# Optimization experiments

Measured on AMD Instinct MI355X. Metric: run time of the kernel, lower is better.

Reference implementation:

```python
import jax, jax.numpy as jnp
import numpy as np

D_MODEL = 512
N_HEADS = 8
D_K = D_MODEL // N_HEADS
D_FF = 2048
N = 4096
EPS = 1e-5


def _layer_norm(x, g, b):
    mu = jnp.mean(x, axis=-1, keepdims=True)
    var = jnp.mean(jnp.square(x - mu), axis=-1, keepdims=True)
    return (x - mu) * jax.lax.rsqrt(var + EPS) * g + b


def setup_inputs() -> dict:
    key = jax.random.key(0)
    ks = jax.random.split(key, 16)
    s = 1.0 / np.sqrt(D_MODEL)
    sf = 1.0 / np.sqrt(D_FF)
    inp = {
        "h": jax.random.normal(ks[0], (N, D_MODEL), dtype=jnp.float32),
        "adj": jax.random.randint(ks[1], (N, N), 0, 2, dtype=jnp.int32),
        "Wq": jax.random.uniform(ks[2], (D_MODEL, D_MODEL), jnp.float32, -s, s),
        "bq": jnp.zeros((D_MODEL,), jnp.float32),
        "Wk": jax.random.uniform(ks[3], (D_MODEL, D_MODEL), jnp.float32, -s, s),
        "bk": jnp.zeros((D_MODEL,), jnp.float32),
        "Wv": jax.random.uniform(ks[4], (D_MODEL, D_MODEL), jnp.float32, -s, s),
        "bv": jnp.zeros((D_MODEL,), jnp.float32),
        "Wo": jax.random.uniform(ks[5], (D_MODEL, D_MODEL), jnp.float32, -s, s),
        "bo": jnp.zeros((D_MODEL,), jnp.float32),
        "W1": jax.random.uniform(ks[6], (D_FF, D_MODEL), jnp.float32, -s, s),
        "b1": jnp.zeros((D_FF,), jnp.float32),
        "W2": jax.random.uniform(ks[7], (D_MODEL, D_FF), jnp.float32, -sf, sf),
        "b2": jnp.zeros((D_MODEL,), jnp.float32),
        "ln1_g": jnp.ones((D_MODEL,), jnp.float32),
        "ln1_b": jnp.zeros((D_MODEL,), jnp.float32),
        "ln2_g": jnp.ones((D_MODEL,), jnp.float32),
        "ln2_b": jnp.zeros((D_MODEL,), jnp.float32),
    }
    return inp


def reference(h, adj, Wq, bq, Wk, bk, Wv, bv, Wo, bo, W1, b1, W2, b2,
              ln1_g, ln1_b, ln2_g, ln2_b):
    n = h.shape[0]
    # adjacency + self loops, used as attention mask (batch=1)
    mask = adj.astype(jnp.float32) + jnp.eye(n, dtype=jnp.float32)  # [N,N]

    # QKV projections, split into heads: [N, H, Dk]
    q = (h @ Wq.T + bq).reshape(n, N_HEADS, D_K)
    k = (h @ Wk.T + bk).reshape(n, N_HEADS, D_K)
    v = (h @ Wv.T + bv).reshape(n, N_HEADS, D_K)

    scores = jnp.einsum("nhd,mhd->hnm", q, k) / jnp.sqrt(jnp.float32(D_K))
    scores = jnp.where(mask[None, :, :] == 0, jnp.float32(-1e9), scores)
    attn = jax.nn.softmax(scores, axis=-1)  # dropout is identity in eval
    ctx = jnp.einsum("hnm,mhd->nhd", attn, v).reshape(n, D_MODEL)
    attn_out = ctx @ Wo.T + bo

    h1 = _layer_norm(h + attn_out, ln1_g, ln1_b)
    ff = jax.nn.relu(h1 @ W1.T + b1) @ W2.T + b2
    h2 = _layer_norm(h1 + ff, ln2_g, ln2_b)
    return h2
```

## Files before the change

### kernel.cpp

```cpp
#include <hip/hip_runtime.h>
#include <stdint.h>
#include <stddef.h>

typedef __bf16 bf16;
typedef __bf16 bf16x8 __attribute__((ext_vector_type(8)));
typedef float  f32x4  __attribute__((ext_vector_type(4)));

typedef __attribute__((address_space(3))) void       lds_void;
typedef __attribute__((address_space(1))) const void gbl_cvoid;

#define ASYNC_CP16(g, l) \
  __builtin_amdgcn_global_load_lds((gbl_cvoid*)(g), (lds_void*)(l), 16, 0, 0)

__device__ __forceinline__ int swz(int r) { return (r & 7) ^ ((r & 8) >> 1); }

struct CastArgs {
  const float* src[7];
  bf16*        dst[7];
  int          cum[8];
};

__global__ __launch_bounds__(256) void k_prep(
    const int* __restrict__ adj, unsigned long long* __restrict__ mb,
    CastArgs a, int total8)
{
  const int bid = blockIdx.x;
  if (bid < 65536) {
    const int gw   = (int)(((unsigned)bid * 256 + threadIdx.x) >> 6);
    const int lane = threadIdx.x & 63;
    const int av   = adj[(size_t)gw * 64 + lane];
    unsigned long long m = __ballot(av != 0);
    const int row = gw >> 6, wc = gw & 63;
    if ((row >> 6) == wc) m |= 1ull << (row & 63);
    if (lane == 0) mb[gw] = m;
  } else {
    const int g = (bid - 65536) * 256 + threadIdx.x;
    if (g >= total8) return;
    int t = 0;
    while (a.cum[t + 1] <= g) ++t;
    const int i = g - a.cum[t];
    const float4* s = (const float4*)(a.src[t]) + (size_t)i * 2;
    const float4 x0 = s[0], x1 = s[1];
    bf16x8 y;
    y[0] = (bf16)x0.x; y[1] = (bf16)x0.y; y[2] = (bf16)x0.z; y[3] = (bf16)x0.w;
    y[4] = (bf16)x1.x; y[5] = (bf16)x1.y; y[6] = (bf16)x1.z; y[7] = (bf16)x1.w;
    *(bf16x8*)(a.dst[t] + (size_t)i * 8) = y;
  }
}

template <int MT>
__device__ __forceinline__ void gemm_core_async(
    const bf16* __restrict__ A, const bf16* __restrict__ B,
    bf16* As, bf16* Bs, f32x4 (&acc)[4][(MT == 128) ? 4 : 2],
    int K, int m0, int n0, int kbeg, int kend)
{
  constexpr int FN = (MT == 128) ? 4 : 2;
  constexpr int IA = MT / 32;
  const int tid    = threadIdx.x;
  const int lane   = tid & 63;
  const int wave   = tid >> 6;
  const int lane15 = lane & 15;
  const int quad   = lane >> 4;
  const int wm     = (MT == 128) ? ((wave & 1) << 6) : 0;
  const int wn     = (MT == 128) ? ((wave >> 1) << 6) : (wave << 5);

  int srA[IA], soA[IA], srB[4], soB[4];
#pragma unroll
  for (int i = 0; i < IA; ++i) {
    int c  = ((wave * IA + i) << 6) + lane;
    srA[i] = c >> 3;
    soA[i] = ((c & 7) ^ swz(srA[i])) * 8;
  }
#pragma unroll
  for (int i = 0; i < 4; ++i) {
    int c  = ((wave * 4 + i) << 6) + lane;
    srB[i] = c >> 3;
    soB[i] = ((c & 7) ^ swz(srB[i])) * 8;
  }

  const bf16* Ab = A + (size_t)m0 * K;
  const bf16* Bb = B + (size_t)n0 * K;

  for (int k0 = kbeg; k0 < kend; k0 += 64) {
#pragma unroll
    for (int i = 0; i < IA; ++i)
      ASYNC_CP16(Ab + (size_t)srA[i] * K + k0 + soA[i], &As[(wave * IA + i) * 512]);
#pragma unroll
    for (int i = 0; i < 4; ++i)
      ASYNC_CP16(Bb + (size_t)srB[i] * K + k0 + soB[i], &Bs[(wave * 4 + i) * 512]);
    __syncthreads();

#pragma unroll
    for (int kk = 0; kk < 2; ++kk) {
      bf16x8 af[4], bfr[FN];
#pragma unroll
      for (int f = 0; f < 4; ++f) {
        const int ra = wm + f * 16 + lane15;
        af[f] = *(const bf16x8*)&As[ra * 64 + (((kk * 4 + quad) ^ swz(ra)) * 8)];
      }
#pragma unroll
      for (int f = 0; f < FN; ++f) {
        const int rb = wn + f * 16 + lane15;
        bfr[f] = *(const bf16x8*)&Bs[rb * 64 + (((kk * 4 + quad) ^ swz(rb)) * 8)];
      }
#pragma unroll
      for (int fm = 0; fm < 4; ++fm)
#pragma unroll
        for (int fn = 0; fn < FN; ++fn)
          acc[fm][fn] = __builtin_amdgcn_mfma_f32_16x16x32_bf16(
              af[fm], bfr[fn], acc[fm][fn], 0, 0, 0);
    }
    __syncthreads();
  }
}

__global__ __launch_bounds__(256, 2) void k_gemm(
    const bf16* __restrict__ A, const bf16* __restrict__ B,
    const float* __restrict__ bias, bf16* __restrict__ C,
    int N, int K, int relu)
{
  __shared__ __align__(16) bf16 As[128 * 64];
  __shared__ __align__(16) bf16 Bs[128 * 64];
  const int m0 = blockIdx.x * 128, n0 = blockIdx.y * 128;
  f32x4 acc[4][4] = {};
  gemm_core_async<128>(A, B, As, Bs, acc, K, m0, n0, 0, K);

  const int lane15 = threadIdx.x & 15;
  const int quad   = (threadIdx.x & 63) >> 4;
  const int wave   = threadIdx.x >> 6;
  const int wm = (wave & 1) << 6, wn = (wave >> 1) << 6;
#pragma unroll
  for (int fm = 0; fm < 4; ++fm)
#pragma unroll
    for (int fn = 0; fn < 4; ++fn) {
      const int col = n0 + wn + fn * 16 + lane15;
      const float bv = bias[col];
#pragma unroll
      for (int r = 0; r < 4; ++r) {
        const int row = m0 + wm + fm * 16 + quad * 4 + r;
        float v = acc[fm][fn][r] + bv;
        if (relu) v = fmaxf(v, 0.0f);
        C[(size_t)row * N + col] = (bf16)v;
      }
    }
}

__global__ __launch_bounds__(256, 4) void k_gemm_qkv(
    const bf16* __restrict__ h, const bf16* __restrict__ Wcat,
    const float* __restrict__ bq, const float* __restrict__ bk,
    const float* __restrict__ bv,
    bf16* __restrict__ q, bf16* __restrict__ k, bf16* __restrict__ vt)
{
  __shared__ __align__(16) bf16 SM[64 * 64 + 128 * 64];
  bf16* As = SM;
  bf16* Bs = SM + 64 * 64;
  const int m0 = blockIdx.x * 64, n0 = blockIdx.y * 128;
  f32x4 acc[4][2] = {};
  gemm_core_async<64>(h, Wcat, As, Bs, acc, 512, m0, n0, 0, 512);

  const int lane15 = threadIdx.x & 15;
  const int quad   = (threadIdx.x & 63) >> 4;
  const int wave   = threadIdx.x >> 6;
  const int wn     = wave << 5;
  const int proj   = n0 >> 9;
  const int ncol0  = n0 & 511;
  const float* bias = (proj == 0) ? bq : (proj == 1) ? bk : bv;

  if (proj < 2) {
    bf16* C = proj ? k : q;
#pragma unroll
    for (int fm = 0; fm < 4; ++fm)
#pragma unroll
      for (int fn = 0; fn < 2; ++fn) {
        const int col = ncol0 + wn + fn * 16 + lane15;
        const float bvv = bias[col];
#pragma unroll
        for (int r = 0; r < 4; ++r) {
          const int row = m0 + fm * 16 + quad * 4 + r;
          C[(size_t)row * 512 + col] = (bf16)(acc[fm][fn][r] + bvv);
        }
      }
  } else {
    __syncthreads();
#pragma unroll
    for (int fm = 0; fm < 4; ++fm)
#pragma unroll
      for (int fn = 0; fn < 2; ++fn) {
        const int colL = wn + fn * 16 + lane15;
        const float bvv = bias[ncol0 + colL];
#pragma unroll
        for (int r = 0; r < 4; ++r) {
          const int rowL = fm * 16 + quad * 4 + r;
          SM[colL * 72 + rowL] = (bf16)(acc[fm][fn][r] + bvv);
        }
      }
    __syncthreads();
#pragma unroll
    for (int i = 0; i < 4; ++i) {
      const int c = i * 256 + threadIdx.x;
      const int colL = c >> 3, rw = (c & 7) * 8;
      *(bf16x8*)&vt[(size_t)(ncol0 + colL) * 4096 + m0 + rw] =
          *(const bf16x8*)&SM[colL * 72 + rw];
    }
  }
}

__global__ __launch_bounds__(256, 4) void k_gemm_sk(
    const bf16* __restrict__ A, const bf16* __restrict__ B,
    float* __restrict__ Cp, int N, int K, int Ksplit)
{
  __shared__ __align__(16) bf16 As[64 * 64];
  __shared__ __align__(16) bf16 Bs[128 * 64];
  const int m0 = blockIdx.x * 64, n0 = blockIdx.y * 128;
  const int kbeg = blockIdx.z * Ksplit;
  f32x4 acc[4][2] = {};
  gemm_core_async<64>(A, B, As, Bs, acc, K, m0, n0, kbeg, kbeg + Ksplit);

  const int lane15 = threadIdx.x & 15;
  const int quad   = (threadIdx.x & 63) >> 4;
  const int wave   = threadIdx.x >> 6;
  const int wn     = wave << 5;
  float* Cz = Cp + (size_t)blockIdx.z * 4096 * N;
#pragma unroll
  for (int fm = 0; fm < 4; ++fm)
#pragma unroll
    for (int fn = 0; fn < 2; ++fn) {
      const int col = n0 + wn + fn * 16 + lane15;
#pragma unroll
      for (int r = 0; r < 4; ++r) {
        const int row = m0 + fm * 16 + quad * 4 + r;
        Cz[(size_t)row * N + col] = acc[fm][fn][r];
      }
    }
}

__global__ __launch_bounds__(256, 4) void k_attn(
    const bf16* __restrict__ Q, const bf16* __restrict__ Km,
    const bf16* __restrict__ Vt, const unsigned long long* __restrict__ mb,
    bf16* __restrict__ Opart, float* __restrict__ Lpart)
{
  constexpr int PP = 68;
  __shared__ __align__(16) bf16 Ks[64 * 64];
  __shared__ __align__(16) bf16 Vs[64 * 64];
  __shared__ __align__(16) bf16 Plb[4][32 * PP];

  const int tid    = threadIdx.x;
  const int wave   = tid >> 6;
  const int lane   = tid & 63;
  const int lane15 = lane & 15;
  const int quad   = lane >> 4;
  const int sp     = blockIdx.x & 3;
  const int hd     = (blockIdx.x >> 2) & 7;
  const int qt     = blockIdx.x >> 5;
  const int qrow   = qt * 128 + wave * 32;

  bf16x8 qf[2][2];
#pragma unroll
  for (int mt = 0; mt < 2; ++mt)
#pragma unroll
    for (int c = 0; c < 2; ++c)
      qf[mt][c] = *(const bf16x8*)&Q[(size_t)(qrow + mt * 16 + lane15) * 512 +
                                     hd * 64 + c * 32 + quad * 8];

  int srK[2], soK[2];
#pragma unroll
  for (int i = 0; i < 2; ++i) {
    int c  = ((wave * 2 + i) << 6) + lane;
    srK[i] = c >> 3;
    soK[i] = ((c & 7) ^ swz(srK[i])) * 8;
  }
  const bf16* KmB[2] = {
      Km + (size_t)srK[0] * 512 + hd * 64 + soK[0],
      Km + (size_t)srK[1] * 512 + hd * 64 + soK[1]};
  const bf16* VtB[2] = {
      Vt + (size_t)(hd * 64 + srK[0]) * 4096 + soK[0],
      Vt + (size_t)(hd * 64 + srK[1]) * 4096 + soK[1]};

  bf16x8 ones;
#pragma unroll
  for (int j = 0; j < 8; ++j) ones[j] = (bf16)1.0f;

  f32x4 o[2][4] = {};
  f32x4 la[2]   = {};

  const int kt0 = sp * 16;
#pragma unroll
  for (int i = 0; i < 2; ++i)
    ASYNC_CP16(KmB[i] + (size_t)(kt0 * 64) * 512, &Ks[(wave * 2 + i) * 512]);
  __syncthreads();

  for (int kt = kt0; kt < kt0 + 16; ++kt) {
    const int kb = kt * 64;

#pragma unroll
    for (int i = 0; i < 2; ++i)
      ASYNC_CP16(VtB[i] + kb, &Vs[(wave * 2 + i) * 512]);

    unsigned long long mw[2][4];
#pragma unroll
    for (int mt = 0; mt < 2; ++mt)
#pragma unroll
      for (int r = 0; r < 4; ++r)
        mw[mt][r] = mb[(size_t)(qrow + mt * 16 + quad * 4 + r) * 64 + kt] >> lane15;

#pragma unroll
    for (int g = 0; g < 4; ++g) {
      const int row = g * 16 + lane15;
      bf16x8 k0f = *(const bf16x8*)&Ks[row * 64 + ((quad       ^ swz(row)) * 8)];
      bf16x8 k1f = *(const bf16x8*)&Ks[row * 64 + (((4 + quad) ^ swz(row)) * 8)];
#pragma unroll
      for (int mt = 0; mt < 2; ++mt) {
        f32x4 s = {};
        __builtin_amdgcn_s_setprio(1);
        s = __builtin_amdgcn_mfma_f32_16x16x32_bf16(qf[mt][0], k0f, s, 0, 0, 0);
        s = __builtin_amdgcn_mfma_f32_16x16x32_bf16(qf[mt][1], k1f, s, 0, 0, 0);
        __builtin_amdgcn_s_setprio(0);
#pragma unroll
        for (int r = 0; r < 4; ++r) {
          const bool ok = ((mw[mt][r] >> (g * 16)) & 1ull) != 0;
          const float p = ok ? __expf(s[r] * 0.125f) : 0.0f;
          Plb[wave][(mt * 16 + quad * 4 + r) * PP + g * 16 + lane15] = (bf16)p;
        }
      }
    }
    __syncthreads();

    if (kt + 1 < kt0 + 16) {
      const int kb2 = (kt + 1) * 64;
#pragma unroll
      for (int i = 0; i < 2; ++i)
        ASYNC_CP16(KmB[i] + (size_t)kb2 * 512, &Ks[(wave * 2 + i) * 512]);
    }

#pragma unroll
    for (int c2 = 0; c2 < 2; ++c2) {
      bf16x8 vf[4];
#pragma unroll
      for (int g2 = 0; g2 < 4; ++g2) {
        const int row = g2 * 16 + lane15;
        vf[g2] = *(const bf16x8*)&Vs[row * 64 + (((c2 * 4 + quad) ^ swz(row)) * 8)];
      }
#pragma unroll
      for (int mt = 0; mt < 2; ++mt) {
        bf16x8 pa = *(const bf16x8*)&Plb[wave][(mt * 16 + lane15) * PP + c2 * 32 + quad * 8];
        __builtin_amdgcn_s_setprio(1);
        la[mt] = __builtin_amdgcn_mfma_f32_16x16x32_bf16(pa, ones, la[mt], 0, 0, 0);
#pragma unroll
        for (int g2 = 0; g2 < 4; ++g2)
          o[mt][g2] = __builtin_amdgcn_mfma_f32_16x16x32_bf16(pa, vf[g2], o[mt][g2], 0, 0, 0);
        __builtin_amdgcn_s_setprio(0);
      }
    }
    __syncthreads();
  }

  bf16* Oz = Opart + (size_t)sp * 4096 * 512;
#pragma unroll
  for (int mt = 0; mt < 2; ++mt) {
#pragma unroll
    for (int g2 = 0; g2 < 4; ++g2)
#pragma unroll
      for (int r = 0; r < 4; ++r) {
        const int row = qrow + mt * 16 + quad * 4 + r;
        Oz[(size_t)row * 512 + hd * 64 + g2 * 16 + lane15] = (bf16)o[mt][g2][r];
      }
    if (lane15 == 0) {
#pragma unroll
      for (int r = 0; r < 4; ++r)
        Lpart[sp * 32768 + (qrow + mt * 16 + quad * 4 + r) * 8 + hd] = la[mt][r];
    }
  }
}

__global__ __launch_bounds__(256) void k_attn_combine(
    const bf16* __restrict__ Opart, const float* __restrict__ Lpart,
    bf16* __restrict__ ctx)
{
  const int g = blockIdx.x * 256 + threadIdx.x;
  const size_t base = (size_t)g * 8;
  const int row = g >> 6;
  const int hd  = (g & 63) >> 3;
  float acc[8] = {};
  float l = 0.0f;
#pragma unroll
  for (int s = 0; s < 4; ++s) {
    bf16x8 ov = *(const bf16x8*)&Opart[(size_t)s * 4096 * 512 + base];
#pragma unroll
    for (int j = 0; j < 8; ++j) acc[j] += (float)ov[j];
    l += Lpart[s * 32768 + row * 8 + hd];
  }
  const float rl = 1.0f / l;
  bf16x8 y;
#pragma unroll
  for (int j = 0; j < 8; ++j) y[j] = (bf16)(acc[j] * rl);
  *(bf16x8*)(ctx + base) = y;
}

template <int F32OUT>
__global__ __launch_bounds__(256) void k_addln_sk(
    const bf16* __restrict__ x, const float* __restrict__ Cp,
    const float* __restrict__ bias,
    const float* __restrict__ gam, const float* __restrict__ bet,
    void* __restrict__ out)
{
  const int wave = threadIdx.x >> 6, lane = threadIdx.x & 63;
  const int row  = blockIdx.x * 4 + wave;
  const size_t base = (size_t)row * 512 + lane * 8;
  const int col = lane * 8;
  bf16x8 xv = *(const bf16x8*)(x + base);
  const float* p0 = Cp + base;
  const float* p1 = Cp + (size_t)4096 * 512 + base;
  f32x4 a0 = *(const f32x4*)p0, a1 = *(const f32x4*)(p0 + 4);
  f32x4 b0 = *(const f32x4*)p1, b1 = *(const f32x4*)(p1 + 4);
  f32x4 c0 = *(const f32x4*)(bias + col), c1 = *(const f32x4*)(bias + col + 4);
  float v[8], s = 0.0f, s2 = 0.0f;
#pragma unroll
  for (int j = 0; j < 4; ++j) {
    v[j]     = (float)xv[j]     + a0[j] + b0[j] + c0[j];
    v[4 + j] = (float)xv[4 + j] + a1[j] + b1[j] + c1[j];
  }
#pragma unroll
  for (int j = 0; j < 8; ++j) { s += v[j]; s2 += v[j] * v[j]; }
#pragma unroll
  for (int d = 1; d < 64; d <<= 1) { s += __shfl_xor(s, d, 64); s2 += __shfl_xor(s2, d, 64); }
  const float mu  = s * (1.0f / 512.0f);
  const float var = s2 * (1.0f / 512.0f) - mu * mu;
  const float rs  = rsqrtf(var + 1e-5f);
  f32x4 g0 = *(const f32x4*)(gam + col), g1 = *(const f32x4*)(gam + col + 4);
  f32x4 e0 = *(const f32x4*)(bet + col), e1 = *(const f32x4*)(bet + col + 4);
  if (F32OUT) {
    float* o = (float*)out + base;
#pragma unroll
    for (int j = 0; j < 4; ++j) {
      o[j]     = ((v[j] - mu) * rs) * g0[j] + e0[j];
      o[4 + j] = ((v[4 + j] - mu) * rs) * g1[j] + e1[j];
    }
  } else {
    bf16x8 ov;
#pragma unroll
    for (int j = 0; j < 4; ++j) {
      ov[j]     = (bf16)(((v[j] - mu) * rs) * g0[j] + e0[j]);
      ov[4 + j] = (bf16)(((v[4 + j] - mu) * rs) * g1[j] + e1[j]);
    }
    *(bf16x8*)((bf16*)out + base) = ov;
  }
}

extern "C" void kernel_launch(void* const* d_in, const int* in_sizes, int n_in,
                              void* d_out, int out_size, void* d_ws, size_t ws_size,
                              hipStream_t stream)
{
  const int*   adj = (const int*)  d_in[1];
  const float* bq  = (const float*)d_in[3];
  const float* bk  = (const float*)d_in[5];
  const float* bv  = (const float*)d_in[7];
  const float* bo  = (const float*)d_in[9];
  const float* b1  = (const float*)d_in[11];
  const float* b2  = (const float*)d_in[13];
  const float* g1  = (const float*)d_in[14];
  const float* be1 = (const float*)d_in[15];
  const float* g2  = (const float*)d_in[16];
  const float* be2 = (const float*)d_in[17];

  char* ws = (char*)d_ws;
  const size_t MB = 1024 * 1024;

  bf16* hb  = (bf16*)(ws + 0 * MB);
  bf16* Wqb = (bf16*)(ws + 4 * MB);
  bf16* Wkb = (bf16*)(ws + 4 * MB + 512 * 1024);
  bf16* Wvb = (bf16*)(ws + 5 * MB);
  bf16* Wob = (bf16*)(ws + 5 * MB + 512 * 1024);
  bf16* W1b = (bf16*)(ws + 6 * MB);
  bf16* W2b = (bf16*)(ws + 8 * MB);

  bf16* q    = (bf16*)(ws + 12 * MB);
  bf16* k    = (bf16*)(ws + 16 * MB);
  bf16* vt   = (bf16*)(ws + 24 * MB);
  unsigned long long* mbits = (unsigned long long*)(ws + 28 * MB);
  bf16* ctx  = (bf16*)(ws + 30 * MB);
  bf16*  Opart = (bf16*)(ws + 34 * MB);
  float* Lpart = (float*)(ws + 50 * MB);
  float* skP   = (float*)(ws + 34 * MB);
  bf16* h1   = (bf16*)(ws + 12 * MB);
  bf16* ff1  = (bf16*)(ws + 16 * MB);

  CastArgs ca;
  const int srcIdx[7] = {0, 2, 4, 6, 8, 10, 12};
  bf16* dsts[7] = {hb, Wqb, Wkb, Wvb, Wob, W1b, W2b};
  int cum = 0;
  for (int t = 0; t < 7; ++t) {
    ca.src[t] = (const float*)d_in[srcIdx[t]];
    ca.dst[t] = dsts[t];
    ca.cum[t] = cum;
    cum += in_sizes[srcIdx[t]] / 8;
  }
  ca.cum[7] = cum;

  const dim3 blk(256);

  k_prep<<<dim3(65536 + (cum + 255) / 256), blk, 0, stream>>>(adj, mbits, ca, cum);
  k_gemm_qkv<<<dim3(64, 12), blk, 0, stream>>>(hb, Wqb, bq, bk, bv, q, k, vt);
  k_attn<<<dim3(1024), blk, 0, stream>>>(q, k, vt, mbits, Opart, Lpart);
  k_attn_combine<<<dim3(1024), blk, 0, stream>>>(Opart, Lpart, ctx);
  k_gemm_sk<<<dim3(64, 4, 2), blk, 0, stream>>>(ctx, Wob, skP, 512, 512, 256);
  k_addln_sk<0><<<dim3(1024), blk, 0, stream>>>(hb, skP, bo, g1, be1, (void*)h1);
  k_gemm<<<dim3(32, 16), blk, 0, stream>>>(h1, W1b, b1, ff1, 2048, 512, 1);
  k_gemm_sk<<<dim3(64, 4, 2), blk, 0, stream>>>(ff1, W2b, skP, 512, 2048, 1024);
  k_addln_sk<1><<<dim3(1024), blk, 0, stream>>>(h1, skP, b2, g2, be2, d_out);
}
```

Before: 294.0 us.

## Restructure attention K/V loading, prefetch mask bits, swizzle P tile, coalesce output

Reworks the attention inner loop so that K and V tiles are loaded together at the top of each iteration, followed by one barrier. The mask words for the next tile are prefetched into registers while the current tile is computed. The P scratch tile now uses a row pitch of 72 plus an XOR swizzle to avoid LDS bank conflicts, and exp is computed with exp2 and a folded scale. The output is staged through LDS so each lane writes 16-byte vectors instead of scattered bf16 stores. The cost is that the K load is no longer overlapped with the PV MFMAs, and more registers are held live for the mask prefetch.

```diff
diff --git a/kernel.cpp b/kernel.cpp
--- a/kernel.cpp
+++ b/kernel.cpp
@@ -239,7 +239,7 @@
     const bf16* __restrict__ Vt, const unsigned long long* __restrict__ mb,
     bf16* __restrict__ Opart, float* __restrict__ Lpart)
 {
-  constexpr int PP = 68;
+  constexpr int PP = 72;
   __shared__ __align__(16) bf16 Ks[64 * 64];
   __shared__ __align__(16) bf16 Vs[64 * 64];
   __shared__ __align__(16) bf16 Plb[4][32 * PP];
@@ -284,24 +284,31 @@
   f32x4 la[2]   = {};
 
   const int kt0 = sp * 16;
-#pragma unroll
-  for (int i = 0; i < 2; ++i)
-    ASYNC_CP16(KmB[i] + (size_t)(kt0 * 64) * 512, &Ks[(wave * 2 + i) * 512]);
-  __syncthreads();
+
+  unsigned long long mwc[2][4], mwn[2][4] = {};
+#pragma unroll
+  for (int mt = 0; mt < 2; ++mt)
+#pragma unroll
+    for (int r = 0; r < 4; ++r)
+      mwc[mt][r] = mb[(size_t)(qrow + mt * 16 + quad * 4 + r) * 64 + kt0] >> lane15;
 
   for (int kt = kt0; kt < kt0 + 16; ++kt) {
     const int kb = kt * 64;
-
-#pragma unroll
-    for (int i = 0; i < 2; ++i)
-      ASYNC_CP16(VtB[i] + kb, &Vs[(wave * 2 + i) * 512]);
-
-    unsigned long long mw[2][4];
-#pragma unroll
-    for (int mt = 0; mt < 2; ++mt)
-#pragma unroll
-      for (int r = 0; r < 4; ++r)
-        mw[mt][r] = mb[(size_t)(qrow + mt * 16 + quad * 4 + r) * 64 + kt] >> lane15;
+#pragma unroll
+    for (int i = 0; i < 2; ++i) {
+      ASYNC_CP16(KmB[i] + (size_t)kb * 512, &Ks[(wave * 2 + i) * 512]);
+      ASYNC_CP16(VtB[i] + kb,               &Vs[(wave * 2 + i) * 512]);
+    }
+    __syncthreads();
+
+    if (kt + 1 < kt0 + 16) {
+#pragma unroll
+      for (int mt = 0; mt < 2; ++mt)
+#pragma unroll
+        for (int r = 0; r < 4; ++r)
+          mwn[mt][r] =
+              mb[(size_t)(qrow + mt * 16 + quad * 4 + r) * 64 + kt + 1] >> lane15;
+    }
 
 #pragma unroll
     for (int g = 0; g < 4; ++g) {
@@ -317,19 +324,13 @@
         __builtin_amdgcn_s_setprio(0);
 #pragma unroll
         for (int r = 0; r < 4; ++r) {
-          const bool ok = ((mw[mt][r] >> (g * 16)) & 1ull) != 0;
-          const float p = ok ? __expf(s[r] * 0.125f) : 0.0f;
-          Plb[wave][(mt * 16 + quad * 4 + r) * PP + g * 16 + lane15] = (bf16)p;
+          const bool ok = ((mwc[mt][r] >> (g * 16)) & 1ull) != 0;
+          const float p =
+              ok ? __builtin_amdgcn_exp2f(s[r] * 0.18033688f) : 0.0f;
+          Plb[wave][(mt * 16 + quad * 4 + r) * PP +
+                    ((g * 16 + lane15) ^ (quad << 3))] = (bf16)p;
         }
       }
-    }
-    __syncthreads();
-
-    if (kt + 1 < kt0 + 16) {
-      const int kb2 = (kt + 1) * 64;
-#pragma unroll
-      for (int i = 0; i < 2; ++i)
-        ASYNC_CP16(KmB[i] + (size_t)kb2 * 512, &Ks[(wave * 2 + i) * 512]);
     }
 
 #pragma unroll
@@ -342,7 +343,8 @@
       }
 #pragma unroll
       for (int mt = 0; mt < 2; ++mt) {
-        bf16x8 pa = *(const bf16x8*)&Plb[wave][(mt * 16 + lane15) * PP + c2 * 32 + quad * 8];
+        bf16x8 pa = *(const bf16x8*)&Plb[wave][(mt * 16 + lane15) * PP +
+                        ((c2 * 32 + quad * 8) ^ ((lane15 >> 2) << 3))];
         __builtin_amdgcn_s_setprio(1);
         la[mt] = __builtin_amdgcn_mfma_f32_16x16x32_bf16(pa, ones, la[mt], 0, 0, 0);
 #pragma unroll
@@ -351,24 +353,38 @@
         __builtin_amdgcn_s_setprio(0);
       }
     }
+
+#pragma unroll
+    for (int mt = 0; mt < 2; ++mt)
+#pragma unroll
+      for (int r = 0; r < 4; ++r) mwc[mt][r] = mwn[mt][r];
     __syncthreads();
   }
 
+#pragma unroll
+  for (int mt = 0; mt < 2; ++mt)
+#pragma unroll
+    for (int g2 = 0; g2 < 4; ++g2)
+#pragma unroll
+      for (int r = 0; r < 4; ++r)
+        Plb[wave][(mt * 16 + quad * 4 + r) * PP +
+                  ((g2 * 16 + lane15) ^ (quad << 3))] = (bf16)o[mt][g2][r];
+
   bf16* Oz = Opart + (size_t)sp * 4096 * 512;
 #pragma unroll
-  for (int mt = 0; mt < 2; ++mt) {
-#pragma unroll
-    for (int g2 = 0; g2 < 4; ++g2)
-#pragma unroll
-      for (int r = 0; r < 4; ++r) {
-        const int row = qrow + mt * 16 + quad * 4 + r;
-        Oz[(size_t)row * 512 + hd * 64 + g2 * 16 + lane15] = (bf16)o[mt][g2][r];
-      }
-    if (lane15 == 0) {
+  for (int p = 0; p < 4; ++p) {
+    const int rowL = p * 8 + (lane >> 3);
+    const int cw   = (lane & 7) * 8;
+    *(bf16x8*)&Oz[(size_t)(qrow + rowL) * 512 + hd * 64 + cw] =
+        *(const bf16x8*)&Plb[wave][rowL * PP + (cw ^ (((rowL >> 2) & 3) << 3))];
+  }
+
+  if (lane15 == 0) {
+#pragma unroll
+    for (int mt = 0; mt < 2; ++mt)
 #pragma unroll
       for (int r = 0; r < 4; ++r)
         Lpart[sp * 32768 + (qrow + mt * 16 + quad * 4 + r) * 8 + hd] = la[mt][r];
-    }
   }
 }
 
```

Result: slower. 307.1 us (+4.5%).

## Double-buffer K/V tiles and double query rows per wave in attention

Applied to the files above, without the earlier changes.

The attention kernel now double-buffers K and V tiles in LDS, prefetching the next tile before computing the current one, and drops one block barrier per iteration. Each wave handles 64 query rows instead of 32, halving the grid and reusing each loaded K/V tile for twice as many queries. The exponential is computed with a native exp2 and a prescaled constant. In exchange, registers and LDS per block grow, so the occupancy hint drops from 4 blocks to 2 per CU, and the smaller grid may leave less latency hiding.

```diff
diff --git a/kernel.cpp b/kernel.cpp
--- a/kernel.cpp
+++ b/kernel.cpp
@@ -234,15 +234,15 @@
     }
 }
 
-__global__ __launch_bounds__(256, 4) void k_attn(
+__global__ __launch_bounds__(256, 2) void k_attn(
     const bf16* __restrict__ Q, const bf16* __restrict__ Km,
     const bf16* __restrict__ Vt, const unsigned long long* __restrict__ mb,
     bf16* __restrict__ Opart, float* __restrict__ Lpart)
 {
-  constexpr int PP = 68;
-  __shared__ __align__(16) bf16 Ks[64 * 64];
-  __shared__ __align__(16) bf16 Vs[64 * 64];
-  __shared__ __align__(16) bf16 Plb[4][32 * PP];
+  constexpr int PP = 72;
+  __shared__ __align__(16) bf16 Ks[2][64 * 64];
+  __shared__ __align__(16) bf16 Vs[2][64 * 64];
+  __shared__ __align__(16) bf16 Plb[4][64 * PP];
 
   const int tid    = threadIdx.x;
   const int wave   = tid >> 6;
@@ -252,11 +252,11 @@
   const int sp     = blockIdx.x & 3;
   const int hd     = (blockIdx.x >> 2) & 7;
   const int qt     = blockIdx.x >> 5;
-  const int qrow   = qt * 128 + wave * 32;
-
-  bf16x8 qf[2][2];
-#pragma unroll
-  for (int mt = 0; mt < 2; ++mt)
+  const int qrow   = qt * 256 + wave * 64;
+
+  bf16x8 qf[4][2];
+#pragma unroll
+  for (int mt = 0; mt < 4; ++mt)
 #pragma unroll
     for (int c = 0; c < 2; ++c)
       qf[mt][c] = *(const bf16x8*)&Q[(size_t)(qrow + mt * 16 + lane15) * 512 +
@@ -280,36 +280,44 @@
 #pragma unroll
   for (int j = 0; j < 8; ++j) ones[j] = (bf16)1.0f;
 
-  f32x4 o[2][4] = {};
-  f32x4 la[2]   = {};
+  f32x4 o[4][4] = {};
+  f32x4 la[4]   = {};
 
   const int kt0 = sp * 16;
-#pragma unroll
-  for (int i = 0; i < 2; ++i)
-    ASYNC_CP16(KmB[i] + (size_t)(kt0 * 64) * 512, &Ks[(wave * 2 + i) * 512]);
+
+#pragma unroll
+  for (int i = 0; i < 2; ++i) {
+    ASYNC_CP16(KmB[i] + (size_t)(kt0 * 64) * 512, &Ks[0][(wave * 2 + i) * 512]);
+    ASYNC_CP16(VtB[i] + kt0 * 64,                 &Vs[0][(wave * 2 + i) * 512]);
+  }
   __syncthreads();
 
   for (int kt = kt0; kt < kt0 + 16; ++kt) {
-    const int kb = kt * 64;
-
-#pragma unroll
-    for (int i = 0; i < 2; ++i)
-      ASYNC_CP16(VtB[i] + kb, &Vs[(wave * 2 + i) * 512]);
-
-    unsigned long long mw[2][4];
-#pragma unroll
-    for (int mt = 0; mt < 2; ++mt)
+    const int cur = (kt - kt0) & 1;
+
+    if (kt + 1 < kt0 + 16) {
+      const int kb2 = (kt + 1) * 64;
+#pragma unroll
+      for (int i = 0; i < 2; ++i) {
+        ASYNC_CP16(KmB[i] + (size_t)kb2 * 512, &Ks[cur ^ 1][(wave * 2 + i) * 512]);
+        ASYNC_CP16(VtB[i] + kb2,               &Vs[cur ^ 1][(wave * 2 + i) * 512]);
+      }
+    }
+
+    unsigned long long mwc[4][4];
+#pragma unroll
+    for (int mt = 0; mt < 4; ++mt)
 #pragma unroll
       for (int r = 0; r < 4; ++r)
-        mw[mt][r] = mb[(size_t)(qrow + mt * 16 + quad * 4 + r) * 64 + kt] >> lane15;
+        mwc[mt][r] = mb[(size_t)(qrow + mt * 16 + quad * 4 + r) * 64 + kt] >> lane15;
 
 #pragma unroll
     for (int g = 0; g < 4; ++g) {
       const int row = g * 16 + lane15;
-      bf16x8 k0f = *(const bf16x8*)&Ks[row * 64 + ((quad       ^ swz(row)) * 8)];
-      bf16x8 k1f = *(const bf16x8*)&Ks[row * 64 + (((4 + quad) ^ swz(row)) * 8)];
-#pragma unroll
-      for (int mt = 0; mt < 2; ++mt) {
+      bf16x8 k0f = *(const bf16x8*)&Ks[cur][row * 64 + ((quad       ^ swz(row)) * 8)];
+      bf16x8 k1f = *(const bf16x8*)&Ks[cur][row * 64 + (((4 + quad) ^ swz(row)) * 8)];
+#pragma unroll
+      for (int mt = 0; mt < 4; ++mt) {
         f32x4 s = {};
         __builtin_amdgcn_s_setprio(1);
         s = __builtin_amdgcn_mfma_f32_16x16x32_bf16(qf[mt][0], k0f, s, 0, 0, 0);
@@ -317,20 +325,12 @@
         __builtin_amdgcn_s_setprio(0);
 #pragma unroll
         for (int r = 0; r < 4; ++r) {
-          const bool ok = ((mw[mt][r] >> (g * 16)) & 1ull) != 0;
-          const float p = ok ? __expf(s[r] * 0.125f) : 0.0f;
+          const bool ok = ((mwc[mt][r] >> (g * 16)) & 1ull) != 0;
+          const float p = ok ? __builtin_amdgcn_exp2f(s[r] * 0.18033688f) : 0.0f;
           Plb[wave][(mt * 16 + quad * 4 + r) * PP + g * 16 + lane15] = (bf16)p;
         }
       }
     }
-    __syncthreads();
-
-    if (kt + 1 < kt0 + 16) {
-      const int kb2 = (kt + 1) * 64;
-#pragma unroll
-      for (int i = 0; i < 2; ++i)
-        ASYNC_CP16(KmB[i] + (size_t)kb2 * 512, &Ks[(wave * 2 + i) * 512]);
-    }
 
 #pragma unroll
     for (int c2 = 0; c2 < 2; ++c2) {
@@ -338,10 +338,10 @@
 #pragma unroll
       for (int g2 = 0; g2 < 4; ++g2) {
         const int row = g2 * 16 + lane15;
-        vf[g2] = *(const bf16x8*)&Vs[row * 64 + (((c2 * 4 + quad) ^ swz(row)) * 8)];
-      }
-#pragma unroll
-      for (int mt = 0; mt < 2; ++mt) {
+        vf[g2] = *(const bf16x8*)&Vs[cur][row * 64 + (((c2 * 4 + quad) ^ swz(row)) * 8)];
+      }
+#pragma unroll
+      for (int mt = 0; mt < 4; ++mt) {
         bf16x8 pa = *(const bf16x8*)&Plb[wave][(mt * 16 + lane15) * PP + c2 * 32 + quad * 8];
         __builtin_amdgcn_s_setprio(1);
         la[mt] = __builtin_amdgcn_mfma_f32_16x16x32_bf16(pa, ones, la[mt], 0, 0, 0);
@@ -356,7 +356,7 @@
 
   bf16* Oz = Opart + (size_t)sp * 4096 * 512;
 #pragma unroll
-  for (int mt = 0; mt < 2; ++mt) {
+  for (int mt = 0; mt < 4; ++mt) {
 #pragma unroll
     for (int g2 = 0; g2 < 4; ++g2)
 #pragma unroll
@@ -500,7 +500,7 @@
 
   k_prep<<<dim3(65536 + (cum + 255) / 256), blk, 0, stream>>>(adj, mbits, ca, cum);
   k_gemm_qkv<<<dim3(64, 12), blk, 0, stream>>>(hb, Wqb, bq, bk, bv, q, k, vt);
-  k_attn<<<dim3(1024), blk, 0, stream>>>(q, k, vt, mbits, Opart, Lpart);
+  k_attn<<<dim3(512), blk, 0, stream>>>(q, k, vt, mbits, Opart, Lpart);
   k_attn_combine<<<dim3(1024), blk, 0, stream>>>(Opart, Lpart, ctx);
   k_gemm_sk<<<dim3(64, 4, 2), blk, 0, stream>>>(ctx, Wob, skP, 512, 512, 256);
   k_addln_sk<0><<<dim3(1024), blk, 0, stream>>>(hb, skP, bo, g1, be1, (void*)h1);
```

Result: no change. 295.7 us (+0.6%).
